# Optimization experiments

Hardware: AMD Instinct MI355X
Metric: run time of the kernel (lower is better)

## Reference

```python
import jax, jax.numpy as jnp
from jax import lax
import numpy as np

NUM_STEPS = 20
GATE_TIME = 1.0
DT = GATE_TIME / NUM_STEPS
BATCH = 8388608  # number of qubit states (columns)


def setup_inputs() -> dict:
    key = jax.random.key(0)
    k1, k2 = jax.random.split(key)
    # learnable pulse amplitudes, initialized to 2.0 as in the torch module
    amplitudes = jnp.full((NUM_STEPS,), 2.0, dtype=jnp.float32)
    state_real = jax.random.normal(k1, (2, BATCH), dtype=jnp.float32)
    state_imag = jax.random.normal(k2, (2, BATCH), dtype=jnp.float32)
    return {"amplitudes": amplitudes, "state_real": state_real, "state_imag": state_imag}


def reference(amplitudes, state_real, state_imag):
    # H_k = (a_k / 2) * X ;  U_k = exp(-i * H_k * dt) = cos(a_k*dt/2) I - i sin(a_k*dt/2) X
    # (exact closed form of matrix_exp for the Pauli-X generator)
    state = state_real + 1j * state_imag  # [2, B] complex64

    def step(s, a):
        theta = a * (DT * 0.5)
        c = jnp.cos(theta)
        sn = jnp.sin(theta)
        # X @ s swaps the two rows
        s_new = c * s - 1j * sn * s[::-1, :]
        return s_new, None

    state, _ = lax.scan(step, state, amplitudes)
    # return real-valued view [2(real/imag), 2, B]
    return jnp.stack([state.real, state.imag])
```

## Files before the change

kernel.cpp:

```cpp
#include <hip/hip_runtime.h>


typedef float f4 __attribute__((ext_vector_type(4)));

__global__ __launch_bounds__(256) void grape_kernel(
    const float* __restrict__ amps, int nsteps,
    const float* __restrict__ sreal, const float* __restrict__ simag,
    float* __restrict__ out, long long B, long long blocks_per_half) {
    float theta = 0.0f;
    for (int k = 0; k < nsteps; ++k) theta += amps[k];
    theta *= (1.0f / (float)nsteps) * 0.5f;
    const float c = cosf(theta);
    const float s = sinf(theta);

    const long long h = (blockIdx.x >= blocks_per_half) ? 1 : 0;
    const long long v = ((long long)blockIdx.x - h * blocks_per_half) * blockDim.x
                        + threadIdx.x;
    const long long j = v * 4;

    const float* __restrict__ x = sreal + h * B;
    const float* __restrict__ y = simag + (1 - h) * B;
    float* __restrict__ outr = out + h * B;
    float* __restrict__ outi = out + (3 - h) * B;

    if (j + 3 < B) {
        const f4 xv = *(const f4*)(x + j);
        const f4 yv = *(const f4*)(y + j);
        *(f4*)(outr + j) = c * xv + s * yv;
        *(f4*)(outi + j) = c * yv - s * xv;
    } else if (j < B) {
        for (long long t = j; t < B; ++t) {
            const float xs = x[t], ys = y[t];
            outr[t] = c * xs + s * ys;
            outi[t] = c * ys - s * xs;
        }
    }
}

extern "C" void kernel_launch(void* const* d_in, const int* in_sizes, int n_in,
                              void* d_out, int out_size, void* d_ws, size_t ws_size,
                              hipStream_t stream) {
    const float* amps  = (const float*)d_in[0];
    const float* sreal = (const float*)d_in[1];
    const float* simag = (const float*)d_in[2];
    float* out = (float*)d_out;

    int nsteps = in_sizes[0];
    long long B = (long long)in_sizes[1] / 2;

    const int block = 256;
    long long nv = (B + 3) / 4;
    long long blocks_per_half = (nv + block - 1) / block;
    long long grid = 2 * blocks_per_half;

    grape_kernel<<<(dim3)(unsigned)grid, block, 0, stream>>>(
        amps, nsteps, sreal, simag, out, B, blocks_per_half);
}
```

Baseline: 240.2 us.

## Use persistent grid-stride kernel with interleaved halves and 2x unrolled loads

Replaces the one-thread-per-vector launch with a fixed 2048-block grid-stride loop. Even and odd blocks handle the two state halves, and each iteration issues two independent f4 load pairs to raise memory-level parallelism. This removes per-block launch and scheduling overhead and the repeated per-block amplitude reduction, at the cost of relying on 2048 blocks to saturate bandwidth.

```diff
diff --git a/kernel.cpp b/kernel.cpp
--- a/kernel.cpp
+++ b/kernel.cpp
@@ -6,34 +6,50 @@
 __global__ __launch_bounds__(256) void grape_kernel(
     const float* __restrict__ amps, int nsteps,
     const float* __restrict__ sreal, const float* __restrict__ simag,
-    float* __restrict__ out, long long B, long long blocks_per_half) {
+    float* __restrict__ out, long long B) {
     float theta = 0.0f;
     for (int k = 0; k < nsteps; ++k) theta += amps[k];
     theta *= (1.0f / (float)nsteps) * 0.5f;
     const float c = cosf(theta);
     const float s = sinf(theta);
 
-    const long long h = (blockIdx.x >= blocks_per_half) ? 1 : 0;
-    const long long v = ((long long)blockIdx.x - h * blocks_per_half) * blockDim.x
-                        + threadIdx.x;
-    const long long j = v * 4;
+    const int h = (int)(blockIdx.x & 1);
+    const long long tph = ((long long)(gridDim.x >> 1)) * blockDim.x;
+    const long long t0 =
+        ((long long)(blockIdx.x >> 1)) * blockDim.x + threadIdx.x;
 
-    const float* __restrict__ x = sreal + h * B;
-    const float* __restrict__ y = simag + (1 - h) * B;
-    float* __restrict__ outr = out + h * B;
-    float* __restrict__ outi = out + (3 - h) * B;
+    const float* __restrict__ x = sreal + (long long)h * B;
+    const float* __restrict__ y = simag + (long long)(1 - h) * B;
+    float* __restrict__ outr = out + (long long)h * B;
+    float* __restrict__ outi = out + (long long)(3 - h) * B;
 
-    if (j + 3 < B) {
+    const long long nv = B >> 2;
+    long long v = t0;
+
+    for (; v + tph < nv; v += 2 * tph) {
+        const long long j0 = v << 2;
+        const long long j1 = (v + tph) << 2;
+        const f4 x0 = *(const f4*)(x + j0);
+        const f4 y0 = *(const f4*)(y + j0);
+        const f4 x1 = *(const f4*)(x + j1);
+        const f4 y1 = *(const f4*)(y + j1);
+        *(f4*)(outr + j0) = c * x0 + s * y0;
+        *(f4*)(outi + j0) = c * y0 - s * x0;
+        *(f4*)(outr + j1) = c * x1 + s * y1;
+        *(f4*)(outi + j1) = c * y1 - s * x1;
+    }
+    for (; v < nv; v += tph) {
+        const long long j = v << 2;
         const f4 xv = *(const f4*)(x + j);
         const f4 yv = *(const f4*)(y + j);
         *(f4*)(outr + j) = c * xv + s * yv;
         *(f4*)(outi + j) = c * yv - s * xv;
-    } else if (j < B) {
-        for (long long t = j; t < B; ++t) {
-            const float xs = x[t], ys = y[t];
-            outr[t] = c * xs + s * ys;
-            outi[t] = c * ys - s * xs;
-        }
+    }
+
+    for (long long t = (nv << 2) + t0; t < B; t += tph) {
+        const float xs = x[t], ys = y[t];
+        outr[t] = c * xs + s * ys;
+        outi[t] = c * ys - s * xs;
     }
 }
 
@@ -49,10 +65,7 @@
     long long B = (long long)in_sizes[1] / 2;
 
     const int block = 256;
-    long long nv = (B + 3) / 4;
-    long long blocks_per_half = (nv + block - 1) / block;
-    long long grid = 2 * blocks_per_half;
+    const int grid = 2048;
 
-    grape_kernel<<<(dim3)(unsigned)grid, block, 0, stream>>>(
-        amps, nsteps, sreal, simag, out, B, blocks_per_half);
+    grape_kernel<<<grid, block, 0, stream>>>(amps, nsteps, sreal, simag, out, B);
 }
```

New measurement: 242.1 us. About the same (+0.8%).
